# Performance work log

Measured on AMD Instinct MI355X. Metric: run time of the kernel, lower is better.

## Reference

```python
import jax, jax.numpy as jnp
import numpy as np


def _conv3x3(x, w, b):
    # x: [B,C,H,W], w: [O,C,3,3], b: [O]; stride 1, padding 1 (SAME)
    y = jax.lax.conv_general_dilated(
        x, w,
        window_strides=(1, 1),
        padding=((1, 1), (1, 1)),
        dimension_numbers=("NCHW", "OIHW", "NCHW"),
    )
    return y + b[None, :, None, None]


def setup_inputs() -> dict:
    key = jax.random.key(0)
    k_x, k_w1, k_b1, k_w2, k_b2 = jax.random.split(key, 5)
    B, Cin, H, W = 16, 128, 96, 96
    Ch = 256
    # Kaiming-ish small init for conv weights
    x = jax.random.normal(k_x, (B, Cin, H, W), dtype=jnp.float32)
    w1 = jax.random.normal(k_w1, (Ch, Cin, 3, 3), dtype=jnp.float32) * (1.0 / np.sqrt(Cin * 9))
    b1 = jax.random.normal(k_b1, (Ch,), dtype=jnp.float32) * 0.01
    w2 = jax.random.normal(k_w2, (2, Ch, 3, 3), dtype=jnp.float32) * (1.0 / np.sqrt(Ch * 9))
    b2 = jax.random.normal(k_b2, (2,), dtype=jnp.float32) * 0.01
    return {"x": x, "w1": w1, "b1": b1, "w2": w2, "b2": b2}


def reference(x, w1, b1, w2, b2):
    # DeformConv2d with zero offsets == plain 3x3 conv (stride 1, pad 1) + bias.
    h = jax.nn.relu(_conv3x3(x, w1, b1))  # [B,256,H,W]
    return _conv3x3(h, w2, b2)            # [B,2,H,W]
```

## Files before the change

kernel.cpp:

```cpp
#include <hip/hip_runtime.h>
#include <stdint.h>

typedef unsigned short ushort_t;
typedef __attribute__((ext_vector_type(8))) short short8;
typedef __attribute__((ext_vector_type(4))) float floatx4;
typedef __attribute__((ext_vector_type(4))) unsigned short ushortx4;
typedef __attribute__((ext_vector_type(8))) unsigned short ushortx8;

#define B_   16
#define CIN  128
#define CH   256
#define HW   96
#define HP   98

#define XPAD_ELEMS (B_*HP*HP*CIN)
#define HPAD_ELEMS (B_*HP*HP*CH)
#define XPAD_OFF 0
#define HPAD_OFF (XPAD_ELEMS*2)
#define W1T_OFF  (HPAD_OFF + HPAD_ELEMS*2)
#define W2T_OFF  (W1T_OFF + 256*1152*2)

__device__ __forceinline__ ushort_t f2bf(float f){
  uint32_t u = __float_as_uint(f);
  u += 0x7FFF + ((u >> 16) & 1);
  return (ushort_t)(u >> 16);
}
__device__ __forceinline__ float bf2f(ushort_t h){
  return __uint_as_float(((uint32_t)h) << 16);
}
__device__ __forceinline__ void async_ld16(void* lds, const void* g){
  __builtin_amdgcn_global_load_lds(
      (const __attribute__((address_space(1))) void*)g,
      (__attribute__((address_space(3))) void*)lds, 16, 0, 0);
}

__global__ void zero_border(uint32_t* __restrict__ base, int C2){
  int tid = blockIdx.x*256 + threadIdx.x;
  int perimg = 388*C2;
  int total = B_*perimg;
  if (tid >= total) return;
  int b = tid / perimg; int r = tid % perimg;
  int cell = r / C2;    int cu = r % C2;
  int y, x;
  if      (cell < 98)  { y = 0;            x = cell;       }
  else if (cell < 196) { y = 97;           x = cell - 98;  }
  else if (cell < 292) { y = cell - 195;   x = 0;          }
  else                 { y = cell - 291;   x = 97;         }
  base[((b*HP + y)*HP + x)*C2 + cu] = 0u;
}

__global__ void transform_x(const float* __restrict__ x, ushort_t* __restrict__ xpad){
  __shared__ float lds[32][33];
  int bid = blockIdx.x;
  int ct = bid & 3; int xt = (bid>>2) % 3; int yt = (bid/12) % 24; int b = bid/288;
  int c0 = ct*32, x0 = xt*32, y0 = yt*4;
  int t = threadIdx.x;
  for (int yy=0; yy<4; ++yy){
    int y = y0 + yy;
    #pragma unroll
    for (int rep=0; rep<4; ++rep){
      int idx = rep*256 + t;
      int ci = idx >> 5, xj = idx & 31;
      lds[ci][xj] = x[((b*CIN + c0+ci)*HW + y)*HW + x0 + xj];
    }
    __syncthreads();
    int px = t >> 3, quad = t & 7;
    ushortx4 v;
    #pragma unroll
    for (int k=0;k<4;k++) v[k] = f2bf(lds[quad*4+k][px]);
    *(ushortx4*)&xpad[(((b*HP + y+1)*HP) + x0+px+1)*CIN + c0 + quad*4] = v;
    __syncthreads();
  }
}

__global__ void transform_w1(const float* __restrict__ w1, ushort_t* __restrict__ w1t){
  int tid = blockIdx.x*256 + threadIdx.x;
  int o = tid / 1152, k = tid - o*1152;
  int tap = k >> 7, c = k & 127;
  w1t[tid] = f2bf(w1[(o*CIN + c)*9 + tap]);
}

__global__ void transform_w2(const float* __restrict__ w2, float* __restrict__ w2t){
  int tid = blockIdx.x*256 + threadIdx.x;
  if (tid >= 4608) return;
  int ch = tid & 1, c = (tid >> 1) & 255, tap = tid >> 9;
  w2t[tid] = w2[(ch*CH + c)*9 + tap];
}

#define C1_TILE(KT, VMN, SA, SB) { \
  asm volatile("s_waitcnt vmcnt(" #VMN ")" ::: "memory"); \
  __builtin_amdgcn_s_barrier(); \
  __builtin_amdgcn_sched_barrier(0); \
  const int kt_ = (KT); \
  const ushort_t* Ab = &Alds[(kt_ & 1) * 16384]; \
  const ushort_t* Bb = &Blds[(kt_ % 3) * 12288]; \
  short8 aa0[4], aa1[4], bb0[3], bb1[3], cc0[4], cc1[4]; \
   \
  _Pragma("unroll") \
  for (int nf=0; nf<3; ++nf) bb0[nf] = *(const short8*)&Bb[bbase_r + nf*1024 + koff0]; \
  _Pragma("unroll") \
  for (int mf=0; mf<4; ++mf) aa0[mf] = *(const short8*)&Ab[abase_r + mf*1024 + koff0]; \
  if (SA) { \
    const int ka_ = kt_ + 1; const int ab_ = (ka_ & 1) * 16384; \
    async_ld16(&Alds[ab_ +     0 + adst], &w1t[asrc +       0 + ka_*64]); \
    async_ld16(&Alds[ab_ +  4096 + adst], &w1t[asrc +   73728 + ka_*64]); \
  } \
  __builtin_amdgcn_s_barrier(); \
  asm volatile("s_waitcnt lgkmcnt(0)" ::: "memory"); \
  __builtin_amdgcn_sched_barrier(0); \
  __builtin_amdgcn_s_setprio(1); \
  _Pragma("unroll") \
  for (int mf=0; mf<4; ++mf) \
    _Pragma("unroll") \
    for (int nf=0; nf<3; ++nf) \
      acc[mf][nf] = __builtin_amdgcn_mfma_f32_16x16x32_bf16(aa0[mf], bb0[nf], acc[mf][nf], 0,0,0); \
  __builtin_amdgcn_s_setprio(0); \
  __builtin_amdgcn_s_barrier(); \
   \
  _Pragma("unroll") \
  for (int mf=0; mf<4; ++mf) aa1[mf] = *(const short8*)&Ab[abase_r + (mf+4)*1024 + koff0]; \
  if (SA) { \
    const int ka_ = kt_ + 1; const int ab_ = (ka_ & 1) * 16384; \
    async_ld16(&Alds[ab_ +  8192 + adst], &w1t[asrc + 2*73728 + ka_*64]); \
    async_ld16(&Alds[ab_ + 12288 + adst], &w1t[asrc + 3*73728 + ka_*64]); \
  } \
  __builtin_amdgcn_s_barrier(); \
  asm volatile("s_waitcnt lgkmcnt(0)" ::: "memory"); \
  __builtin_amdgcn_sched_barrier(0); \
  __builtin_amdgcn_s_setprio(1); \
  _Pragma("unroll") \
  for (int mf=0; mf<4; ++mf) \
    _Pragma("unroll") \
    for (int nf=0; nf<3; ++nf) \
      acc[mf+4][nf] = __builtin_amdgcn_mfma_f32_16x16x32_bf16(aa1[mf], bb0[nf], acc[mf+4][nf], 0,0,0); \
  __builtin_amdgcn_s_setprio(0); \
  __builtin_amdgcn_s_barrier(); \
   \
  _Pragma("unroll") \
  for (int nf=0; nf<3; ++nf) bb1[nf] = *(const short8*)&Bb[bbase_r + nf*1024 + koff1]; \
  _Pragma("unroll") \
  for (int mf=0; mf<4; ++mf) cc0[mf] = *(const short8*)&Ab[abase_r + mf*1024 + koff1]; \
  if (SB) { \
    const int kb_ = kt_ + 2; \
    const int tapb_ = kb_ >> 1; \
    const int dyb_ = tapb_/3; const int dxb_ = tapb_ - dyb_*3; \
    const int bdb_ = (dyb_*HP + dxb_)*CIN + (kb_&1)*64; \
    const int bb_ = (kb_ % 3) * 12288; \
    async_ld16(&Blds[bb_ +    0 + bdst], &xpad[bsrc +            bdb_]); \
    async_ld16(&Blds[bb_ + 4096 + bdst], &xpad[bsrc + 2*HP*CIN + bdb_]); \
  } \
  __builtin_amdgcn_s_barrier(); \
  asm volatile("s_waitcnt lgkmcnt(0)" ::: "memory"); \
  __builtin_amdgcn_sched_barrier(0); \
  __builtin_amdgcn_s_setprio(1); \
  _Pragma("unroll") \
  for (int mf=0; mf<4; ++mf) \
    _Pragma("unroll") \
    for (int nf=0; nf<3; ++nf) \
      acc[mf][nf] = __builtin_amdgcn_mfma_f32_16x16x32_bf16(cc0[mf], bb1[nf], acc[mf][nf], 0,0,0); \
  __builtin_amdgcn_s_setprio(0); \
  __builtin_amdgcn_s_barrier(); \
   \
  _Pragma("unroll") \
  for (int mf=0; mf<4; ++mf) cc1[mf] = *(const short8*)&Ab[abase_r + (mf+4)*1024 + koff1]; \
  if (SB) { \
    const int kb_ = kt_ + 2; \
    const int tapb_ = kb_ >> 1; \
    const int dyb_ = tapb_/3; const int dxb_ = tapb_ - dyb_*3; \
    const int bdb_ = (dyb_*HP + dxb_)*CIN + (kb_&1)*64; \
    const int bb_ = (kb_ % 3) * 12288; \
    async_ld16(&Blds[bb_ + 8192 + bdst], &xpad[bsrc + 4*HP*CIN + bdb_]); \
  } \
  __builtin_amdgcn_s_barrier(); \
  asm volatile("s_waitcnt lgkmcnt(0)" ::: "memory"); \
  __builtin_amdgcn_sched_barrier(0); \
  __builtin_amdgcn_s_setprio(1); \
  _Pragma("unroll") \
  for (int mf=0; mf<4; ++mf) \
    _Pragma("unroll") \
    for (int nf=0; nf<3; ++nf) \
      acc[mf+4][nf] = __builtin_amdgcn_mfma_f32_16x16x32_bf16(cc1[mf], bb1[nf], acc[mf+4][nf], 0,0,0); \
  __builtin_amdgcn_s_setprio(0); \
}

__global__ __launch_bounds__(512, 1) void conv1(const ushort_t* __restrict__ xpad,
                                                const ushort_t* __restrict__ w1t,
                                                const float* __restrict__ b1,
                                                ushort_t* __restrict__ hpad){
  __shared__ __align__(16) ushort_t Alds[2*16384];
  __shared__ __align__(16) ushort_t Blds[3*12288];
  int orig = blockIdx.x;
  int bid = (orig & 7) * 96 + (orig >> 3);
  int b = bid / 48; int rem = bid - b*48;
  int y0 = (rem/3)*6, x0 = (rem - (rem/3)*3)*32;
  int t = threadIdx.x;
  int lane = t & 63, wave = t >> 6;
  int wm = wave & 1, wn = wave >> 1;
  int r = lane & 15, q = lane >> 4;

  const int arow0 = t >> 3;
  const int soct  = (t & 7) ^ (arow0 & 7);
  const int adst  = t * 8;
  const int asrc  = arow0 * 1152 + soct * 8;
  const int bty0  = arow0 >> 5, btx0 = arow0 & 31;
  const int bdst  = t * 8;
  const int bsrc  = ((b*HP + y0 + bty0)*HP + x0 + btx0)*CIN + soct * 8;

  const int koff0 = ((0*4 + q) ^ (r & 7)) * 8;
  const int koff1 = ((1*4 + q) ^ (r & 7)) * 8;
  const int abase_r = (wm*128 + r) * 64;
  const int bbase_r = (wn*48  + r) * 64;

  floatx4 acc[8][3];
  #pragma unroll
  for (int i=0;i<8;i++)
    #pragma unroll
    for (int j=0;j<3;j++) acc[i][j] = (floatx4){0.f,0.f,0.f,0.f};

  #pragma unroll
  for (int j=0;j<3;++j) async_ld16(&Blds[0     + j*4096 + bdst], &xpad[bsrc + j*(2*HP*CIN)]);
  #pragma unroll
  for (int j=0;j<4;++j) async_ld16(&Alds[0     + j*4096 + adst], &w1t[asrc + j*73728]);
  #pragma unroll
  for (int j=0;j<3;++j) async_ld16(&Blds[12288 + j*4096 + bdst], &xpad[bsrc + j*(2*HP*CIN) + 64]);

  for (int kt=0; kt<16; ++kt){
    C1_TILE(kt, 3, 1, 1)
  }
  C1_TILE(16, 3, 1, 0)
  C1_TILE(17, 0, 0, 0)

  #pragma unroll
  for (int mf=0; mf<8; ++mf){
    int o = wm*128 + mf*16 + q*4;
    float bias0 = b1[o], bias1 = b1[o+1], bias2 = b1[o+2], bias3 = b1[o+3];
    #pragma unroll
    for (int nf=0; nf<3; ++nf){
      int n = wn*48 + nf*16 + r;
      int ty = n >> 5, tx = n & 31;
      ushortx4 v;
      v[0] = f2bf(fmaxf(acc[mf][nf][0] + bias0, 0.f));
      v[1] = f2bf(fmaxf(acc[mf][nf][1] + bias1, 0.f));
      v[2] = f2bf(fmaxf(acc[mf][nf][2] + bias2, 0.f));
      v[3] = f2bf(fmaxf(acc[mf][nf][3] + bias3, 0.f));
      *(ushortx4*)&hpad[((b*HP + y0+ty+1)*HP + (x0+tx+1))*CH + o] = v;
    }
  }
}

__global__ __launch_bounds__(256) void conv2(const ushort_t* __restrict__ hpad,
                                             const float* __restrict__ w2t,
                                             const float* __restrict__ b2,
                                             float* __restrict__ out){
  __shared__ __align__(16) ushort_t hlds[25600];
  __shared__ float part[4][64][2];
  int bid = blockIdx.x;
  int b = bid / 144; int rem = bid - b*144;
  int yt = rem / 12, xt = rem - yt*12;
  int y0 = yt*8, x0 = xt*8;
  int t = threadIdx.x;
  int wave = t >> 6, lane = t & 63;

  for (int pass=0; pass<13; ++pass){
    int u = pass*256 + t;
    if (u < 3200){
      int cell = u >> 5, cf = u & 31;
      int hy = cell / 10, hx = cell - hy*10;
      const ushort_t* src = hpad + ((b*HP + y0+hy)*HP + (x0+hx))*CH
                                 + ((cf ^ (cell & 7)) << 3);
      async_ld16(&hlds[(pass*256 + wave*64)*8], src);
    }
  }
  __syncthreads();

  int q = __builtin_amdgcn_readfirstlane(wave);
  int ty = lane >> 3, tx = lane & 7;
  float a0 = 0.f, a1 = 0.f;
  for (int tap=0; tap<9; ++tap){
    int dy = tap/3, dxx = tap - dy*3;
    int cell = (ty+dy)*10 + (tx+dxx);
    int s = cell & 7;
    const float* wp = w2t + (tap*256 + q*64)*2;
    #pragma unroll
    for (int g=0; g<8; ++g){
      int j = q*8 + g;
      ushortx8 hv = *(const ushortx8*)&hlds[cell*256 + ((j ^ s) << 3)];
      #pragma unroll
      for (int i=0;i<8;i++){
        float hf = bf2f(hv[i]);
        a0 = fmaf(hf, wp[(g*8+i)*2    ], a0);
        a1 = fmaf(hf, wp[(g*8+i)*2 + 1], a1);
      }
    }
  }
  part[wave][lane][0] = a0;
  part[wave][lane][1] = a1;
  __syncthreads();
  if (t < 128){
    int sel = t >> 6, pix = t & 63;
    float v = part[0][pix][sel] + part[1][pix][sel]
            + part[2][pix][sel] + part[3][pix][sel] + b2[sel];
    int yy = y0 + (pix >> 3), xx = x0 + (pix & 7);
    out[(b*2 + sel)*9216 + yy*96 + xx] = v;
  }
}

extern "C" void kernel_launch(void* const* d_in, const int* in_sizes, int n_in,
                              void* d_out, int out_size, void* d_ws, size_t ws_size,
                              hipStream_t stream){
  const float* x  = (const float*)d_in[0];
  const float* w1 = (const float*)d_in[1];
  const float* b1 = (const float*)d_in[2];
  const float* w2 = (const float*)d_in[3];
  const float* b2 = (const float*)d_in[4];
  float* out = (float*)d_out;
  char* ws = (char*)d_ws;
  ushort_t* xpad = (ushort_t*)(ws + XPAD_OFF);
  ushort_t* hpad = (ushort_t*)(ws + HPAD_OFF);
  ushort_t* w1t  = (ushort_t*)(ws + W1T_OFF);
  float*    w2t  = (float*)(ws + W2T_OFF);

  hipLaunchKernelGGL(zero_border, dim3(16*388*64/256),  dim3(256), 0, stream, (uint32_t*)xpad, 64);
  hipLaunchKernelGGL(zero_border, dim3(16*388*128/256), dim3(256), 0, stream, (uint32_t*)hpad, 128);
  hipLaunchKernelGGL(transform_x,  dim3(4608),  dim3(256), 0, stream, x, xpad);
  hipLaunchKernelGGL(transform_w1, dim3(1152),  dim3(256), 0, stream, w1, w1t);
  hipLaunchKernelGGL(transform_w2, dim3(18),    dim3(256), 0, stream, w2, w2t);
  hipLaunchKernelGGL(conv1, dim3(768),  dim3(512), 0, stream, xpad, w1t, b1, hpad);
  hipLaunchKernelGGL(conv2, dim3(2304), dim3(256), 0, stream, hpad, w2t, b2, out);
}
```

Baseline: 174.5 us.

## Merge prep kernels, widen transform_x tiles, and remap conv1 waves to 4x2

The zero-border fills and both weight transforms are merged into one prep_small kernel, removing three launches. transform_x now handles all 128 channels per block, one row at a time, and writes 16-byte vectors. conv1's 8 waves go from a 2x4 to a 4x2 M/N layout, each wave owning 64 output channels by 96 pixels, which changes which fragments are reloaded from LDS per k-step. The bigger LDS tile in transform_x may lower its occupancy.

```diff
diff --git a/kernel.cpp b/kernel.cpp
--- a/kernel.cpp
+++ b/kernel.cpp
@@ -34,11 +34,8 @@
       (__attribute__((address_space(3))) void*)lds, 16, 0, 0);
 }
 
-__global__ void zero_border(uint32_t* __restrict__ base, int C2){
-  int tid = blockIdx.x*256 + threadIdx.x;
+__device__ __forceinline__ void zb(uint32_t* base, int C2, int tid){
   int perimg = 388*C2;
-  int total = B_*perimg;
-  if (tid >= total) return;
   int b = tid / perimg; int r = tid % perimg;
   int cell = r / C2;    int cu = r % C2;
   int y, x;
@@ -49,42 +46,55 @@
   base[((b*HP + y)*HP + x)*C2 + cu] = 0u;
 }
 
-__global__ void transform_x(const float* __restrict__ x, ushort_t* __restrict__ xpad){
-  __shared__ float lds[32][33];
+__global__ __launch_bounds__(256) void prep_small(const float* __restrict__ w1,
+                                                  const float* __restrict__ w2,
+                                                  uint32_t* __restrict__ xpadw,
+                                                  uint32_t* __restrict__ hpadw,
+                                                  ushort_t* __restrict__ w1t,
+                                                  float* __restrict__ w2t){
+  int tid = blockIdx.x*256 + threadIdx.x;
+  const int NZX = B_*388*64;
+  const int NZH = B_*388*128;
+  const int NW1 = 256*1152;
+  if (tid < NZX){
+    zb(xpadw, 64, tid);
+  } else if (tid < NZX + NZH){
+    zb(hpadw, 128, tid - NZX);
+  } else if (tid < NZX + NZH + NW1){
+    int r = tid - (NZX + NZH);
+    int o = r / 1152, k = r - o*1152;
+    int tap = k >> 7, c = k & 127;
+    w1t[r] = f2bf(w1[(o*CIN + c)*9 + tap]);
+  } else {
+    int r = tid - (NZX + NZH + NW1);
+    int ch = r & 1, c = (r >> 1) & 255, tap = r >> 9;
+    w2t[r] = w2[(ch*CH + c)*9 + tap];
+  }
+}
+
+__global__ __launch_bounds__(256) void transform_x(const float* __restrict__ x,
+                                                   ushort_t* __restrict__ xpad){
+  __shared__ float lds[128][33];
   int bid = blockIdx.x;
-  int ct = bid & 3; int xt = (bid>>2) % 3; int yt = (bid/12) % 24; int b = bid/288;
-  int c0 = ct*32, x0 = xt*32, y0 = yt*4;
+  int xt = bid % 3; int y = (bid/3) % 96; int b = bid/288;
+  int x0 = xt*32;
   int t = threadIdx.x;
-  for (int yy=0; yy<4; ++yy){
-    int y = y0 + yy;
-    #pragma unroll
-    for (int rep=0; rep<4; ++rep){
-      int idx = rep*256 + t;
-      int ci = idx >> 5, xj = idx & 31;
-      lds[ci][xj] = x[((b*CIN + c0+ci)*HW + y)*HW + x0 + xj];
-    }
-    __syncthreads();
-    int px = t >> 3, quad = t & 7;
-    ushortx4 v;
-    #pragma unroll
-    for (int k=0;k<4;k++) v[k] = f2bf(lds[quad*4+k][px]);
-    *(ushortx4*)&xpad[(((b*HP + y+1)*HP) + x0+px+1)*CIN + c0 + quad*4] = v;
-    __syncthreads();
-  }
-}
-
-__global__ void transform_w1(const float* __restrict__ w1, ushort_t* __restrict__ w1t){
-  int tid = blockIdx.x*256 + threadIdx.x;
-  int o = tid / 1152, k = tid - o*1152;
-  int tap = k >> 7, c = k & 127;
-  w1t[tid] = f2bf(w1[(o*CIN + c)*9 + tap]);
-}
-
-__global__ void transform_w2(const float* __restrict__ w2, float* __restrict__ w2t){
-  int tid = blockIdx.x*256 + threadIdx.x;
-  if (tid >= 4608) return;
-  int ch = tid & 1, c = (tid >> 1) & 255, tap = tid >> 9;
-  w2t[tid] = w2[(ch*CH + c)*9 + tap];
+  #pragma unroll
+  for (int rep=0; rep<16; ++rep){
+    int idx = rep*256 + t;
+    int ci = idx >> 5, xj = idx & 31;
+    lds[ci][xj] = x[((b*CIN + ci)*HW + y)*HW + x0 + xj];
+  }
+  __syncthreads();
+  int px = t & 31, oc = t >> 5;
+  ushort_t* dst = &xpad[((b*HP + y+1)*HP + x0+px+1)*CIN + oc*16];
+  ushortx8 v0, v1;
+  #pragma unroll
+  for (int k=0;k<8;k++) v0[k] = f2bf(lds[oc*16+k][px]);
+  #pragma unroll
+  for (int k=0;k<8;k++) v1[k] = f2bf(lds[oc*16+8+k][px]);
+  *(ushortx8*)dst = v0;
+  *(ushortx8*)(dst+8) = v1;
 }
 
 #define C1_TILE(KT, VMN, SA, SB) { \
@@ -94,7 +104,7 @@
   const int kt_ = (KT); \
   const ushort_t* Ab = &Alds[(kt_ & 1) * 16384]; \
   const ushort_t* Bb = &Blds[(kt_ % 3) * 12288]; \
-  short8 aa0[4], aa1[4], bb0[3], bb1[3], cc0[4], cc1[4]; \
+  short8 aa0[4], cc0[4], bb0[3], bb1[3], dd0[3], dd1[3]; \
    \
   _Pragma("unroll") \
   for (int nf=0; nf<3; ++nf) bb0[nf] = *(const short8*)&Bb[bbase_r + nf*1024 + koff0]; \
@@ -118,7 +128,7 @@
   __builtin_amdgcn_s_barrier(); \
    \
   _Pragma("unroll") \
-  for (int mf=0; mf<4; ++mf) aa1[mf] = *(const short8*)&Ab[abase_r + (mf+4)*1024 + koff0]; \
+  for (int nf=0; nf<3; ++nf) bb1[nf] = *(const short8*)&Bb[bbase_r + (nf+3)*1024 + koff0]; \
   if (SA) { \
     const int ka_ = kt_ + 1; const int ab_ = (ka_ & 1) * 16384; \
     async_ld16(&Alds[ab_ +  8192 + adst], &w1t[asrc + 2*73728 + ka_*64]); \
@@ -132,12 +142,12 @@
   for (int mf=0; mf<4; ++mf) \
     _Pragma("unroll") \
     for (int nf=0; nf<3; ++nf) \
-      acc[mf+4][nf] = __builtin_amdgcn_mfma_f32_16x16x32_bf16(aa1[mf], bb0[nf], acc[mf+4][nf], 0,0,0); \
+      acc[mf][nf+3] = __builtin_amdgcn_mfma_f32_16x16x32_bf16(aa0[mf], bb1[nf], acc[mf][nf+3], 0,0,0); \
   __builtin_amdgcn_s_setprio(0); \
   __builtin_amdgcn_s_barrier(); \
    \
   _Pragma("unroll") \
-  for (int nf=0; nf<3; ++nf) bb1[nf] = *(const short8*)&Bb[bbase_r + nf*1024 + koff1]; \
+  for (int nf=0; nf<3; ++nf) dd0[nf] = *(const short8*)&Bb[bbase_r + nf*1024 + koff1]; \
   _Pragma("unroll") \
   for (int mf=0; mf<4; ++mf) cc0[mf] = *(const short8*)&Ab[abase_r + mf*1024 + koff1]; \
   if (SB) { \
@@ -157,12 +167,12 @@
   for (int mf=0; mf<4; ++mf) \
     _Pragma("unroll") \
     for (int nf=0; nf<3; ++nf) \
-      acc[mf][nf] = __builtin_amdgcn_mfma_f32_16x16x32_bf16(cc0[mf], bb1[nf], acc[mf][nf], 0,0,0); \
+      acc[mf][nf] = __builtin_amdgcn_mfma_f32_16x16x32_bf16(cc0[mf], dd0[nf], acc[mf][nf], 0,0,0); \
   __builtin_amdgcn_s_setprio(0); \
   __builtin_amdgcn_s_barrier(); \
    \
   _Pragma("unroll") \
-  for (int mf=0; mf<4; ++mf) cc1[mf] = *(const short8*)&Ab[abase_r + (mf+4)*1024 + koff1]; \
+  for (int nf=0; nf<3; ++nf) dd1[nf] = *(const short8*)&Bb[bbase_r + (nf+3)*1024 + koff1]; \
   if (SB) { \
     const int kb_ = kt_ + 2; \
     const int tapb_ = kb_ >> 1; \
@@ -179,7 +189,7 @@
   for (int mf=0; mf<4; ++mf) \
     _Pragma("unroll") \
     for (int nf=0; nf<3; ++nf) \
-      acc[mf+4][nf] = __builtin_amdgcn_mfma_f32_16x16x32_bf16(cc1[mf], bb1[nf], acc[mf+4][nf], 0,0,0); \
+      acc[mf][nf+3] = __builtin_amdgcn_mfma_f32_16x16x32_bf16(cc0[mf], dd1[nf], acc[mf][nf+3], 0,0,0); \
   __builtin_amdgcn_s_setprio(0); \
 }
 
@@ -195,7 +205,7 @@
   int y0 = (rem/3)*6, x0 = (rem - (rem/3)*3)*32;
   int t = threadIdx.x;
   int lane = t & 63, wave = t >> 6;
-  int wm = wave & 1, wn = wave >> 1;
+  int wm = wave & 3, wn = wave >> 2;
   int r = lane & 15, q = lane >> 4;
 
   const int arow0 = t >> 3;
@@ -208,14 +218,14 @@
 
   const int koff0 = ((0*4 + q) ^ (r & 7)) * 8;
   const int koff1 = ((1*4 + q) ^ (r & 7)) * 8;
-  const int abase_r = (wm*128 + r) * 64;
-  const int bbase_r = (wn*48  + r) * 64;
-
-  floatx4 acc[8][3];
-  #pragma unroll
-  for (int i=0;i<8;i++)
+  const int abase_r = (wm*64 + r) * 64;
+  const int bbase_r = (wn*96 + r) * 64;
+
+  floatx4 acc[4][6];
+  #pragma unroll
+  for (int i=0;i<4;i++)
     #pragma unroll
-    for (int j=0;j<3;j++) acc[i][j] = (floatx4){0.f,0.f,0.f,0.f};
+    for (int j=0;j<6;j++) acc[i][j] = (floatx4){0.f,0.f,0.f,0.f};
 
   #pragma unroll
   for (int j=0;j<3;++j) async_ld16(&Blds[0     + j*4096 + bdst], &xpad[bsrc + j*(2*HP*CIN)]);
@@ -231,12 +241,12 @@
   C1_TILE(17, 0, 0, 0)
 
   #pragma unroll
-  for (int mf=0; mf<8; ++mf){
-    int o = wm*128 + mf*16 + q*4;
+  for (int mf=0; mf<4; ++mf){
+    int o = wm*64 + mf*16 + q*4;
     float bias0 = b1[o], bias1 = b1[o+1], bias2 = b1[o+2], bias3 = b1[o+3];
     #pragma unroll
-    for (int nf=0; nf<3; ++nf){
-      int n = wn*48 + nf*16 + r;
+    for (int nf=0; nf<6; ++nf){
+      int n = wn*96 + nf*16 + r;
       int ty = n >> 5, tx = n & 31;
       ushortx4 v;
       v[0] = f2bf(fmaxf(acc[mf][nf][0] + bias0, 0.f));
@@ -320,11 +330,9 @@
   ushort_t* w1t  = (ushort_t*)(ws + W1T_OFF);
   float*    w2t  = (float*)(ws + W2T_OFF);
 
-  hipLaunchKernelGGL(zero_border, dim3(16*388*64/256),  dim3(256), 0, stream, (uint32_t*)xpad, 64);
-  hipLaunchKernelGGL(zero_border, dim3(16*388*128/256), dim3(256), 0, stream, (uint32_t*)hpad, 128);
-  hipLaunchKernelGGL(transform_x,  dim3(4608),  dim3(256), 0, stream, x, xpad);
-  hipLaunchKernelGGL(transform_w1, dim3(1152),  dim3(256), 0, stream, w1, w1t);
-  hipLaunchKernelGGL(transform_w2, dim3(18),    dim3(256), 0, stream, w2, w2t);
+  hipLaunchKernelGGL(prep_small,  dim3(5826), dim3(256), 0, stream,
+                     w1, w2, (uint32_t*)xpad, (uint32_t*)hpad, w1t, w2t);
+  hipLaunchKernelGGL(transform_x, dim3(4608), dim3(256), 0, stream, x, xpad);
   hipLaunchKernelGGL(conv1, dim3(768),  dim3(512), 0, stream, xpad, w1t, b1, hpad);
   hipLaunchKernelGGL(conv2, dim3(2304), dim3(256), 0, stream, hpad, w2t, b2, out);
 }
```

After: 160.4 us. 1.09x faster.
